# Kernel optimization log

Measured on AMD Instinct MI355X. Metric: run time of the kernel, lower is better.

Reference implementation:

```python
import jax, jax.numpy as jnp
from jax import lax
import numpy as np

TAU = 10.0      # tauSr == tauRef
THR = 1.0       # theta
WIDTH = 1.0     # tauRho (surrogate width)
SCALE = 1.0     # scaleRho (surrogate scale)
DECAY = float(np.exp(-1.0 / TAU))


@jax.custom_vjp
def _heaviside(v):
    # spike = 1[v >= theta]
    return (v >= THR).astype(v.dtype)

def _heaviside_fwd(v):
    return _heaviside(v), v

def _heaviside_bwd(v, g):
    # SLAYER exponential surrogate pdf: scaleRho/tauRho * exp(-|v-theta|/tauRho)
    return (g * (SCALE / WIDTH) * jnp.exp(-jnp.abs(v - THR) / WIDTH),)

_heaviside.defvjp(_heaviside_fwd, _heaviside_bwd)


def _conv2d(x, w, pad):
    # x: (B, Cin, H, W), w: (Cout, Cin, kh, kw); SLAYER convs have no bias
    return lax.conv_general_dilated(
        x, w, window_strides=(1, 1), padding=[(pad, pad), (pad, pad)],
        dimension_numbers=("NCHW", "OIHW", "NCHW"))


def _sumpool(x, k):
    # SLAYER pool = sum over kxk window (times a learned scalar applied outside)
    B, C, H, W = x.shape
    return x.reshape(B, C, H // k, k, W // k, k).sum(axis=(3, 5))


def _psp(seq):
    # exponential synaptic (PSP) filter along time: s[t] = a*s[t-1] + x[t]
    a = jnp.asarray(DECAY, seq.dtype)
    def step(s, x_t):
        s = a * s + x_t
        return s, s
    _, out = lax.scan(step, jnp.zeros_like(seq[0]), seq)
    return out  # (T, ...)


def _spikes(u):
    # thresholded spiking with decaying refractory feedback (scaleRef=1):
    # v[t] = u[t] - r[t]; s[t] = 1[v >= theta]; r[t+1] = b*(r[t] + theta*s[t])
    b = jnp.asarray(DECAY, u.dtype)
    def step(r, u_t):
        s = _heaviside(u_t - r)
        r_next = b * (r + THR * s)
        return r_next, s
    _, out = lax.scan(step, jnp.zeros_like(u[0]), u)
    return out  # (T, ...)


def _forward(x, conv1_w, conv2_w, lin_w, w_pool1, w_pool2):
    N, T, C, H, W = x.shape  # (64, 100, 2, 32, 32)
    h = _conv2d(x.reshape(N * T, C, H, W), conv1_w, 2)        # (NT, 4, 32, 32)
    h = _sumpool(h, 4) * w_pool1                               # (NT, 4, 8, 8)
    h = h.reshape(N, T, 4, 8, 8).swapaxes(0, 1)                # (T, N, 4, 8, 8)
    s1 = _spikes(_psp(h))                                      # (T, N, 4, 8, 8)
    h2 = _conv2d(s1.reshape(T * N, 4, 8, 8), conv2_w, 1)       # (TN, 8, 8, 8)
    h2 = (_sumpool(h2, 2) * w_pool2).reshape(T, N, 8, 4, 4)    # (T, N, 8, 4, 4)
    s2 = _spikes(_psp(h2))                                     # (T, N, 8, 4, 4)
    # dense = full-spatial conv (2, 8, 4, 4) -> (N, T, 2)
    return jnp.einsum("tnchw,ochw->nto", s2, lin_w)


def setup_inputs() -> dict:
    key = jax.random.key(0)
    ks = jax.random.split(key, 4)
    x = (jax.random.uniform(ks[0], (64, 100, 2, 32, 32)) < 0.1).astype(jnp.float32)
    conv1_w = jax.random.normal(ks[1], (4, 2, 5, 5), jnp.float32) * 0.3
    conv2_w = jax.random.normal(ks[2], (8, 4, 3, 3), jnp.float32) * 0.3
    lin_w = jax.random.normal(ks[3], (2, 8, 4, 4), jnp.float32) * 0.3
    w_pool1 = jnp.float32(1.0 / 16.0)  # 1.1*theta / (16 * 1.1)
    w_pool2 = jnp.float32(1.0 / 4.0)   # 1.1*theta / (4 * 1.1)
    return {"x": x, "conv1_w": conv1_w, "conv2_w": conv2_w, "lin_w": lin_w,
            "w_pool1": w_pool1, "w_pool2": w_pool2}


def reference(x, conv1_w, conv2_w, lin_w, w_pool1, w_pool2):
    return _forward(x, conv1_w, conv2_w, lin_w, w_pool1, w_pool2)
```

## Files before the change

### kernel.cpp

```cpp
#include <hip/hip_runtime.h>


#define DECAY 0.9048374180359595f

#define BAR_LGKM() asm volatile("s_waitcnt lgkmcnt(0)\n\ts_barrier" ::: "memory")
#define FENCE_LGKM() asm volatile("s_waitcnt lgkmcnt(0)" ::: "memory")

__global__ __launch_bounds__(128) void k0_fold(const float* __restrict__ w1,
        const float* __restrict__ w2, const float* __restrict__ wp1,
        const float* __restrict__ wp2, float* __restrict__ wl1,
        float* __restrict__ wl2, float* __restrict__ out) {
    const int tid = threadIdx.x;
    out[blockIdx.x * 128 + tid] = 0.f;
    if (blockIdx.x != 0) return;
    const float p1 = wp1[0], p2 = wp2[0];
    for (int idx = tid; idx < 512; idx += 128) {
        const int f = idx & 7, c = (idx >> 3) & 3, e = (idx >> 5) & 7, cin = idx >> 8;
        const int cc = c * 2 + cin;
        int alo = e - 3; if (alo < 0) alo = 0;
        int ahi = e;     if (ahi > 4) ahi = 4;
        int blo = f - 3; if (blo < 0) blo = 0;
        int bhi = f;     if (bhi > 4) bhi = 4;
        float s = 0.f;
        for (int a = alo; a <= ahi; ++a)
            for (int b = blo; b <= bhi; ++b)
                s += w1[cc * 25 + a * 5 + b];
        wl1[(cin * 8 + e) * 32 + c * 8 + f] = s * p1;
    }
    for (int idx = tid; idx < 512; idx += 128) {
        const int c2 = idx & 7, f = (idx >> 3) & 3, e = (idx >> 5) & 3, cin = idx >> 7;
        int alo = e - 1; if (alo < 0) alo = 0;
        int ahi = e;     if (ahi > 2) ahi = 2;
        int blo = f - 1; if (blo < 0) blo = 0;
        int bhi = f;     if (bhi > 2) bhi = 2;
        float s = 0.f;
        for (int aa = alo; aa <= ahi; ++aa)
            for (int bb = blo; bb <= bhi; ++bb)
                s += w2[((c2 * 4 + cin) * 3 + aa) * 3 + bb];
        wl2[c2 * 68 + cin * 16 + e * 4 + f] = s * p2;
    }
}

__global__ __launch_bounds__(64) void k1(const float* __restrict__ x,
        const float* __restrict__ wg, float* __restrict__ u1) {
    __shared__ __align__(16) float xs[2 * 1296];
    __shared__ __align__(16) float wl[512];
    const int lane = threadIdx.x;
    const int frame = blockIdx.x;
    const int n = frame / 100, t = frame % 100;

    *(float4*)(wl + 4 * lane)       = *(const float4*)(wg + 4 * lane);
    *(float4*)(wl + 256 + 4 * lane) = *(const float4*)(wg + 256 + 4 * lane);

    #pragma unroll
    for (int m0 = 0; m0 < 128; m0 += 64) {
        const int m = m0 + lane;
        if (m < 72) {
            const int cin = m / 36, rem = m % 36;
            const int rr = rem / 9, q4 = rem % 9;
            const int pr = (rr == 0) ? 0 : (rr == 1) ? 9 : (rr == 2) ? 26 : 35;
            *(float4*)(xs + cin * 1296 + pr * 36 + q4 * 4) = make_float4(0.f, 0.f, 0.f, 0.f);
        }
    }
    #pragma unroll
    for (int m0 = 0; m0 < 192; m0 += 64) {
        const int m = m0 + lane;
        if (m < 144) {
            const int cin = m / 72, rem = m % 72;
            const int side = rem & 1, pr = rem >> 1;
            *(float2*)(xs + cin * 1296 + pr * 36 + side * 34) = make_float2(0.f, 0.f);
        }
    }
    const float4* xg = (const float4*)(x + (size_t)frame * 2048);
    #pragma unroll
    for (int q = 0; q < 8; ++q) {
        const int m = q * 64 + lane;
        const float4 v = xg[m];
        const int li = 4 * m;
        const int cin = li >> 10, row = (li >> 5) & 31, col = li & 31;
        const int r = row + 2;
        const int pr = (r & 3) * 9 + (r >> 2);
        float* d = xs + cin * 1296 + pr * 36 + col + 2;
        *(float2*)(d)     = make_float2(v.x, v.y);
        *(float2*)(d + 2) = make_float2(v.z, v.w);
    }
    FENCE_LGKM();

    const int cp = lane >> 5;
    const int i  = (lane >> 2) & 7;
    const int jh = (lane >> 1) & 1;
    const int eh = lane & 1;

    float acc[2][4] = {{0.f, 0.f, 0.f, 0.f}, {0.f, 0.f, 0.f, 0.f}};
    const float* tb = xs + (i + eh) * 36 + jh * 16;
    #pragma unroll
    for (int cin = 0; cin < 2; ++cin) {
        #pragma unroll
        for (int et = 0; et < 4; ++et) {
            const int ro = cin * 1296 + et * 9 * 36;
            float xr[20];
            #pragma unroll
            for (int b = 0; b < 5; ++b)
                *(float4*)(xr + 4 * b) = *(const float4*)(tb + ro + 4 * b);
            float wv[16];
            const float* wp = wl + (cin * 8 + eh * 4 + et) * 32 + cp * 16;
            #pragma unroll
            for (int q = 0; q < 4; ++q)
                *(float4*)(wv + 4 * q) = *(const float4*)(wp + 4 * q);
            #pragma unroll
            for (int cl = 0; cl < 2; ++cl) {
                #pragma unroll
                for (int jj = 0; jj < 4; ++jj) {
                    const int o = 4 * jj;
                    acc[cl][jj] += xr[o]*wv[cl*8]     + xr[o+1]*wv[cl*8+1]
                                 + xr[o+2]*wv[cl*8+2] + xr[o+3]*wv[cl*8+3]
                                 + xr[o+4]*wv[cl*8+4] + xr[o+5]*wv[cl*8+5]
                                 + xr[o+6]*wv[cl*8+6] + xr[o+7]*wv[cl*8+7];
                }
            }
        }
    }
    #pragma unroll
    for (int cl = 0; cl < 2; ++cl)
        #pragma unroll
        for (int jj = 0; jj < 4; ++jj)
            acc[cl][jj] += __shfl_xor(acc[cl][jj], 1);

    const float o0 = eh ? acc[1][0] : acc[0][0];
    const float o1 = eh ? acc[1][1] : acc[0][1];
    const float o2 = eh ? acc[1][2] : acc[0][2];
    const float o3 = eh ? acc[1][3] : acc[0][3];
    *(float4*)(u1 + (size_t)t * 16384 + n * 256 + (2 * cp + eh) * 64 + i * 8 + jh * 4) =
        make_float4(o0, o1, o2, o3);
}

__global__ __launch_bounds__(256) void kf(const float* __restrict__ u1,
        const float* __restrict__ wl2g, const float* __restrict__ lw,
        float* __restrict__ out) {
    __shared__ __align__(16) float ls1[100 * 260];
    __shared__ __align__(16) float ls2[100 * 36];
    const int tid = threadIdx.x;
    const int n = blockIdx.x >> 2, qtr = blockIdx.x & 3;
    const int wave = tid >> 6, l64 = tid & 63;
    const float a = DECAY;

    const float* up = u1 + n * 256 + tid;

    const int sub = tid >> 4, l16 = tid & 15;
    const int c2l = l16 >> 3, i2 = (l16 >> 1) & 3, jhp = l16 & 1;
    const int c2g = qtr * 2 + c2l;

    float4 wreg[16];
    {
        const float* wbase = wl2g + c2g * 68;
        #pragma unroll
        for (int q = 0; q < 16; ++q)
            wreg[q] = *(const float4*)(wbase + (q >> 2) * 16 + (q & 3) * 4);
    }

    float dwA[8], dwB[8];
    {
        const int idx = l64 & 3;
        #pragma unroll
        for (int m = 0; m < 8; ++m) {
            dwA[m] = lw[qtr * 32 + idx * 8 + m];
            dwB[m] = lw[128 + qtr * 32 + idx * 8 + m];
        }
    }

    float vbuf[100];
    #pragma unroll
    for (int k = 0; k < 100; ++k) vbuf[k] = up[(size_t)k * 16384];
    {
        float psp = 0.f, rr = 0.f;
        #pragma unroll
        for (int k = 0; k < 100; ++k) {
            psp = a * psp + vbuf[k];
            const float vv = psp - rr;
            const float s = (vv >= 1.f) ? 1.f : 0.f;
            rr = a * (rr + s);
            ls1[k * 260 + tid] = s;
        }
    }
    BAR_LGKM();

    #pragma unroll 1
    for (int pass = 0; pass < 7; ++pass) {
        const int slot = sub + 16 * pass;
        if (slot < 100) {
            const float* sb = ls1 + slot * 260;
            float acc0 = 0.f, acc1 = 0.f;
            #pragma unroll
            for (int cin = 0; cin < 4; ++cin) {
                #pragma unroll
                for (int e = 0; e < 4; ++e) {
                    const int ri = 2 * i2 + e - 1;
                    const int rc = (ri < 0) ? 0 : (ri > 7 ? 7 : ri);
                    const bool rok = (ri >= 0) && (ri <= 7);
                    float rr8[8];
                    const float* rp = sb + cin * 64 + rc * 8;
                    *(float4*)(rr8)     = *(const float4*)(rp);
                    *(float4*)(rr8 + 4) = *(const float4*)(rp + 4);
                    float xr[6];
                    xr[0] = jhp ? rr8[3] : 0.0f;
                    xr[1] = jhp ? rr8[4] : rr8[0];
                    xr[2] = jhp ? rr8[5] : rr8[1];
                    xr[3] = jhp ? rr8[6] : rr8[2];
                    xr[4] = jhp ? rr8[7] : rr8[3];
                    xr[5] = jhp ? 0.0f   : rr8[4];
                    if (!rok) {
                        #pragma unroll
                        for (int m = 0; m < 6; ++m) xr[m] = 0.0f;
                    }
                    const float4 wf = wreg[cin * 4 + e];
                    acc0 += xr[0] * wf.x; acc0 += xr[1] * wf.y;
                    acc0 += xr[2] * wf.z; acc0 += xr[3] * wf.w;
                    acc1 += xr[2] * wf.x; acc1 += xr[3] * wf.y;
                    acc1 += xr[4] * wf.z; acc1 += xr[5] * wf.w;
                }
            }
            *(float2*)(ls2 + slot * 36 + c2l * 16 + i2 * 4 + 2 * jhp) =
                make_float2(acc0, acc1);
        }
    }
    BAR_LGKM();

    if (wave == 0) {
        if (l64 < 32) {
            float psp2 = 0.f, rr2 = 0.f;
            #pragma unroll
            for (int k = 0; k < 100; ++k) {
                const float u = ls2[k * 36 + l64];
                psp2 = a * psp2 + u;
                const float vv = psp2 - rr2;
                const float s = (vv >= 1.f) ? 1.f : 0.f;
                rr2 = a * (rr2 + s);
                ls2[k * 36 + l64] = s;
            }
        }
        FENCE_LGKM();
        const int idx = l64 & 3;
        #pragma unroll 1
        for (int pass = 0; pass < 7; ++pass) {
            const int slot = (l64 >> 2) + 16 * pass;
            if (slot < 100) {
                float a0 = 0.f, a1 = 0.f;
                #pragma unroll
                for (int m = 0; m < 8; ++m) {
                    const float s = ls2[slot * 36 + idx * 8 + m];
                    a0 += s * dwA[m];
                    a1 += s * dwB[m];
                }
                a0 += __shfl_down(a0, 2); a0 += __shfl_down(a0, 1);
                a1 += __shfl_down(a1, 2); a1 += __shfl_down(a1, 1);
                if (idx == 0) {
                    atomicAdd(&out[n * 200 + slot * 2],     a0);
                    atomicAdd(&out[n * 200 + slot * 2 + 1], a1);
                }
            }
        }
    }
}

extern "C" void kernel_launch(void* const* d_in, const int* in_sizes, int n_in,
                              void* d_out, int out_size, void* d_ws, size_t ws_size,
                              hipStream_t stream) {
    const float* x   = (const float*)d_in[0];
    const float* w1  = (const float*)d_in[1];
    const float* w2  = (const float*)d_in[2];
    const float* lw  = (const float*)d_in[3];
    const float* wp1 = (const float*)d_in[4];
    const float* wp2 = (const float*)d_in[5];

    float* u1  = (float*)d_ws;
    float* wl1 = u1 + 1638400;
    float* wl2 = wl1 + 512;
    float* out = (float*)d_out;

    k0_fold<<<100, 128, 0, stream>>>(w1, w2, wp1, wp2, wl1, wl2, out);
    k1<<<6400, 64, 0, stream>>>(x, wl1, u1);
    kf<<<256, 256, 0, stream>>>(u1, wl2, lw, out);
}
```

Baseline: 119.8 us.

## Reorder folded conv1 weights, read them from global, and make u1 batch-major

```diff
diff --git a/kernel.cpp b/kernel.cpp
--- a/kernel.cpp
+++ b/kernel.cpp
@@ -9,14 +9,13 @@
 __global__ __launch_bounds__(128) void k0_fold(const float* __restrict__ w1,
         const float* __restrict__ w2, const float* __restrict__ wp1,
         const float* __restrict__ wp2, float* __restrict__ wl1,
-        float* __restrict__ wl2, float* __restrict__ out) {
+        float* __restrict__ wl2) {
     const int tid = threadIdx.x;
-    out[blockIdx.x * 128 + tid] = 0.f;
-    if (blockIdx.x != 0) return;
     const float p1 = wp1[0], p2 = wp2[0];
     for (int idx = tid; idx < 512; idx += 128) {
-        const int f = idx & 7, c = (idx >> 3) & 3, e = (idx >> 5) & 7, cin = idx >> 8;
-        const int cc = c * 2 + cin;
+        const int cl = idx & 1, f = (idx >> 1) & 7, cp = (idx >> 4) & 1;
+        const int e = (idx >> 5) & 7, cin = idx >> 8;
+        const int cc = (2 * cp + cl) * 2 + cin;
         int alo = e - 3; if (alo < 0) alo = 0;
         int ahi = e;     if (ahi > 4) ahi = 4;
         int blo = f - 3; if (blo < 0) blo = 0;
@@ -25,7 +24,7 @@
         for (int a = alo; a <= ahi; ++a)
             for (int b = blo; b <= bhi; ++b)
                 s += w1[cc * 25 + a * 5 + b];
-        wl1[(cin * 8 + e) * 32 + c * 8 + f] = s * p1;
+        wl1[idx] = s * p1;
     }
     for (int idx = tid; idx < 512; idx += 128) {
         const int c2 = idx & 7, f = (idx >> 3) & 3, e = (idx >> 5) & 3, cin = idx >> 7;
@@ -42,15 +41,15 @@
 }
 
 __global__ __launch_bounds__(64) void k1(const float* __restrict__ x,
-        const float* __restrict__ wg, float* __restrict__ u1) {
+        const float* __restrict__ wg, float* __restrict__ u1,
+        float* __restrict__ out) {
     __shared__ __align__(16) float xs[2 * 1296];
-    __shared__ __align__(16) float wl[512];
     const int lane = threadIdx.x;
     const int frame = blockIdx.x;
     const int n = frame / 100, t = frame % 100;
 
-    *(float4*)(wl + 4 * lane)       = *(const float4*)(wg + 4 * lane);
-    *(float4*)(wl + 256 + 4 * lane) = *(const float4*)(wg + 256 + 4 * lane);
+    if (blockIdx.x < 50)
+        ((float4*)out)[blockIdx.x * 64 + lane] = make_float4(0.f, 0.f, 0.f, 0.f);
 
     #pragma unroll
     for (int m0 = 0; m0 < 128; m0 += 64) {
@@ -91,7 +90,7 @@
     const int jh = (lane >> 1) & 1;
     const int eh = lane & 1;
 
-    float acc[2][4] = {{0.f, 0.f, 0.f, 0.f}, {0.f, 0.f, 0.f, 0.f}};
+    float2 accp[4] = {{0.f, 0.f}, {0.f, 0.f}, {0.f, 0.f}, {0.f, 0.f}};
     const float* tb = xs + (i + eh) * 36 + jh * 16;
     #pragma unroll
     for (int cin = 0; cin < 2; ++cin) {
@@ -102,35 +101,32 @@
             #pragma unroll
             for (int b = 0; b < 5; ++b)
                 *(float4*)(xr + 4 * b) = *(const float4*)(tb + ro + 4 * b);
-            float wv[16];
-            const float* wp = wl + (cin * 8 + eh * 4 + et) * 32 + cp * 16;
-            #pragma unroll
-            for (int q = 0; q < 4; ++q)
-                *(float4*)(wv + 4 * q) = *(const float4*)(wp + 4 * q);
-            #pragma unroll
-            for (int cl = 0; cl < 2; ++cl) {
+            float4 wt[4];
+            const float4* wp4 = (const float4*)(wg + (cin * 8 + eh * 4 + et) * 32 + cp * 16);
+            #pragma unroll
+            for (int q = 0; q < 4; ++q) wt[q] = wp4[q];
+            const float2* wv2 = (const float2*)wt;
+            #pragma unroll
+            for (int jj = 0; jj < 4; ++jj) {
+                const int o = 4 * jj;
                 #pragma unroll
-                for (int jj = 0; jj < 4; ++jj) {
-                    const int o = 4 * jj;
-                    acc[cl][jj] += xr[o]*wv[cl*8]     + xr[o+1]*wv[cl*8+1]
-                                 + xr[o+2]*wv[cl*8+2] + xr[o+3]*wv[cl*8+3]
-                                 + xr[o+4]*wv[cl*8+4] + xr[o+5]*wv[cl*8+5]
-                                 + xr[o+6]*wv[cl*8+6] + xr[o+7]*wv[cl*8+7];
-                }
-            }
-        }
-    }
-    #pragma unroll
-    for (int cl = 0; cl < 2; ++cl)
-        #pragma unroll
-        for (int jj = 0; jj < 4; ++jj)
-            acc[cl][jj] += __shfl_xor(acc[cl][jj], 1);
-
-    const float o0 = eh ? acc[1][0] : acc[0][0];
-    const float o1 = eh ? acc[1][1] : acc[0][1];
-    const float o2 = eh ? acc[1][2] : acc[0][2];
-    const float o3 = eh ? acc[1][3] : acc[0][3];
-    *(float4*)(u1 + (size_t)t * 16384 + n * 256 + (2 * cp + eh) * 64 + i * 8 + jh * 4) =
+                for (int m = 0; m < 8; ++m) {
+                    accp[jj].x += xr[o + m] * wv2[m].x;
+                    accp[jj].y += xr[o + m] * wv2[m].y;
+                }
+            }
+        }
+    }
+    #pragma unroll
+    for (int jj = 0; jj < 4; ++jj) {
+        accp[jj].x += __shfl_xor(accp[jj].x, 1);
+        accp[jj].y += __shfl_xor(accp[jj].y, 1);
+    }
+    const float o0 = eh ? accp[0].y : accp[0].x;
+    const float o1 = eh ? accp[1].y : accp[1].x;
+    const float o2 = eh ? accp[2].y : accp[2].x;
+    const float o3 = eh ? accp[3].y : accp[3].x;
+    *(float4*)(u1 + (size_t)n * 25600 + t * 256 + (2 * cp + eh) * 64 + i * 8 + jh * 4) =
         make_float4(o0, o1, o2, o3);
 }
 
@@ -144,7 +140,7 @@
     const int wave = tid >> 6, l64 = tid & 63;
     const float a = DECAY;
 
-    const float* up = u1 + n * 256 + tid;
+    const float* up = u1 + (size_t)n * 25600 + tid;
 
     const int sub = tid >> 4, l16 = tid & 15;
     const int c2l = l16 >> 3, i2 = (l16 >> 1) & 3, jhp = l16 & 1;
@@ -170,7 +166,7 @@
 
     float vbuf[100];
     #pragma unroll
-    for (int k = 0; k < 100; ++k) vbuf[k] = up[(size_t)k * 16384];
+    for (int k = 0; k < 100; ++k) vbuf[k] = up[k * 256];
     {
         float psp = 0.f, rr = 0.f;
         #pragma unroll
@@ -277,7 +273,7 @@
     float* wl2 = wl1 + 512;
     float* out = (float*)d_out;
 
-    k0_fold<<<100, 128, 0, stream>>>(w1, w2, wp1, wp2, wl1, wl2, out);
-    k1<<<6400, 64, 0, stream>>>(x, wl1, u1);
+    k0_fold<<<1, 128, 0, stream>>>(w1, w2, wp1, wp2, wl1, wl2);
+    k1<<<6400, 64, 0, stream>>>(x, wl1, u1, out);
     kf<<<256, 256, 0, stream>>>(u1, wl2, lw, out);
 }
```

New measurement: 124.7 us. +4.1%, slower.
